# Optimization experiments

Measured on AMD Instinct MI355X. Metric: run time of the kernel, lower is better.

The kernel has to match this reference:

```python
import jax, jax.numpy as jnp
import numpy as np

R = 32            # voxel resolution
DIM = 240         # channels C
EPS_NORM = 0.0    # module eps
BN_EPS = 1e-5     # torch BatchNorm1d default eps


def setup_inputs() -> dict:
    key = jax.random.key(0)
    k1, k2, k3 = jax.random.split(key, 3)
    B, C, N = 4, DIM, 32768
    features = jax.random.normal(k1, (B, C, N), jnp.float32)
    coords = jax.random.uniform(k2, (B, 3, N), jnp.float32)
    # mlp params: Conv1d(2C -> C, kernel 1) + BatchNorm1d(C)
    w = jax.random.normal(k3, (C, 2 * C), jnp.float32) / np.sqrt(2 * C).astype(np.float32)
    b = jnp.zeros((C,), jnp.float32)
    gamma = jnp.ones((C,), jnp.float32)
    beta = jnp.zeros((C,), jnp.float32)
    return {"features": features, "coords": coords, "w": w, "b": b, "gamma": gamma, "beta": beta}


def _voxelize(features, coords):
    # normalize coords into [0, 1], scale to voxel grid
    nc = coords - coords.mean(axis=2, keepdims=True)                      # [B,3,N]
    scale = jnp.linalg.norm(nc, axis=1, keepdims=True).max(axis=2, keepdims=True) * 2.0 + EPS_NORM
    nc = nc / scale + 0.5
    nc = jnp.clip(nc * R, 0, R - 1)
    vox = jnp.round(nc).astype(jnp.int32)
    pos = vox[:, 0] + vox[:, 1] * R + vox[:, 2] * (R * R)                 # [B,N] flattened voxel id
    R3 = R * R * R

    def per_batch(f, p):
        # f: [C,N], p: [N] -> [2C, R3]; per-voxel max feature + second (min) feature
        mx = jax.ops.segment_max(f.T, p, num_segments=R3)                 # [R3, C]
        mn = jax.ops.segment_min(f.T, p, num_segments=R3)                 # [R3, C]
        cnt = jax.ops.segment_sum(jnp.ones_like(p), p, num_segments=R3)  # [R3]
        mask = (cnt > 0)[:, None]
        mx = jnp.where(mask, mx, 0.0)
        mn = jnp.where(mask, mn, 0.0)
        return jnp.concatenate([mx, mn], axis=1).T                        # [2C, R3]

    fea = jax.vmap(per_batch)(features, pos)                              # [B,2C,R3]
    return fea, nc


def reference(features, coords, w, b, gamma, beta):
    fea, nc = _voxelize(features, coords)
    # 1x1 Conv1d (pointwise GEMM) + BatchNorm1d (training-mode batch stats) + Swish
    y = jnp.einsum('co,bov->bcv', w, fea) + b[None, :, None]
    mean = y.mean(axis=(0, 2), keepdims=True)
    var = y.var(axis=(0, 2), keepdims=True)
    y = gamma[None, :, None] * (y - mean) * jax.lax.rsqrt(var + BN_EPS) + beta[None, :, None]
    y = y * jax.nn.sigmoid(y)
    B, C, _ = features.shape
    return y.reshape(B, C, R, R, R), nc
```

## Files before the change

### kernel.cpp

```cpp
#include <hip/hip_runtime.h>
#include <cstdint>
#include <cstddef>

#define RR 32
#define R3 32768
#define NPT 32768
#define CH 240
#define CH2 480
#define NB 4
#define Y_ELEMS 31457280

typedef __attribute__((ext_vector_type(8))) short short8v;
typedef __attribute__((ext_vector_type(4))) float float4v;

union u8pack { short8v v; unsigned short u[8]; };

static __device__ __forceinline__ float bf2f(unsigned short u) {
  return __uint_as_float(((unsigned int)u) << 16);
}
static __device__ __forceinline__ unsigned short f2bf(float f) {
  unsigned int u = __float_as_uint(f);
  u = (u + 0x7FFFu + ((u >> 16) & 1u)) >> 16;
  return (unsigned short)u;
}

__global__ void k_init(int* __restrict__ cnt, float* __restrict__ stats,
                       const float* __restrict__ w, unsigned short* __restrict__ wfrag) {
  int g = blockIdx.x * 256 + threadIdx.x;
  if (g < NB * R3) cnt[g] = 0;
  if (g < 1024) stats[g] = 0.0f;
  if (g < 14400) {
    int lane = g & 63, t = g >> 6;
    int mg = t / 75, r = t % 75;
    int kc = r / 5, mL = r % 5;
    int m = mg * 5 + mL;
    int ln = lane & 15, q = lane >> 4;
    const float* src = w + (size_t)(m * 16 + ln) * CH2 + kc * 32 + q * 8;
    u8pack pk;
#pragma unroll
    for (int j = 0; j < 8; j++) pk.u[j] = f2bf(src[j]);
    *(short8v*)&wfrag[(size_t)g * 8] = pk.v;
  }
}

__global__ __launch_bounds__(1024) void k_coord_stats(const float* __restrict__ coords,
                                                      float* __restrict__ ms) {
  __shared__ float red[1024];
  __shared__ float mean[3];
  int b = blockIdx.x, t = threadIdx.x;
  const float4* cb4 = (const float4*)(coords + (size_t)b * 3 * NPT);
  float s[3] = {0.f, 0.f, 0.f};
  for (int i = t; i < NPT / 4; i += 1024) {
#pragma unroll
    for (int d = 0; d < 3; d++) {
      float4 v = cb4[d * (NPT / 4) + i];
      s[d] += (v.x + v.y) + (v.z + v.w);
    }
  }
  for (int d = 0; d < 3; d++) {
    red[t] = s[d]; __syncthreads();
    for (int k = 512; k > 0; k >>= 1) { if (t < k) red[t] += red[t + k]; __syncthreads(); }
    if (t == 0) mean[d] = red[0] * (1.0f / NPT);
    __syncthreads();
  }
  float m0 = mean[0], m1 = mean[1], m2 = mean[2];
  float mx = 0.f;
  for (int i = t; i < NPT / 4; i += 1024) {
    float4 x = cb4[i], y = cb4[NPT / 4 + i], z = cb4[2 * (NPT / 4) + i];
    float dx, dy, dz, n;
    dx = x.x - m0; dy = y.x - m1; dz = z.x - m2; n = dx * dx + dy * dy + dz * dz; mx = fmaxf(mx, n);
    dx = x.y - m0; dy = y.y - m1; dz = z.y - m2; n = dx * dx + dy * dy + dz * dz; mx = fmaxf(mx, n);
    dx = x.z - m0; dy = y.z - m1; dz = z.z - m2; n = dx * dx + dy * dy + dz * dz; mx = fmaxf(mx, n);
    dx = x.w - m0; dy = y.w - m1; dz = z.w - m2; n = dx * dx + dy * dy + dz * dz; mx = fmaxf(mx, n);
  }
  red[t] = mx; __syncthreads();
  for (int k = 512; k > 0; k >>= 1) { if (t < k) red[t] = fmaxf(red[t], red[t + k]); __syncthreads(); }
  if (t == 0) {
    ms[b * 4 + 0] = m0; ms[b * 4 + 1] = m1; ms[b * 4 + 2] = m2;
    ms[b * 4 + 3] = sqrtf(red[0]) * 2.0f;
  }
}

__global__ void k_pos_nc(const float* __restrict__ coords, const float* __restrict__ ms,
                         float* __restrict__ ncout, int* __restrict__ pos, int* __restrict__ cnt) {
  int g = blockIdx.x * 256 + threadIdx.x;
  int b = g >> 15, i = g & (NPT - 1);
  const float* cb = coords + (size_t)b * 3 * NPT;
  float scale = ms[b * 4 + 3];
  int vox[3];
#pragma unroll
  for (int d = 0; d < 3; d++) {
    float v = (cb[(size_t)d * NPT + i] - ms[b * 4 + d]) / scale + 0.5f;
    v = fminf(fmaxf(v * (float)RR, 0.0f), (float)(RR - 1));
    ncout[((size_t)(b * 3 + d)) * NPT + i] = v;
    vox[d] = (int)rintf(v);
  }
  int p = (b << 15) | (vox[0] + (vox[1] << 5) + (vox[2] << 10));
  pos[g] = p;
  atomicAdd(&cnt[p], 1);
}

__global__ void k_scan(const int* __restrict__ cnt, int* __restrict__ offs) {
  __shared__ int part[1024];
  int b = blockIdx.x, t = threadIdx.x;
  const int base = b * R3;
  int local[32];
  int s = 0;
#pragma unroll
  for (int j = 0; j < 32; j++) { local[j] = cnt[base + t * 32 + j]; s += local[j]; }
  part[t] = s; __syncthreads();
  for (int d = 1; d < 1024; d <<= 1) {
    int v = (t >= d) ? part[t - d] : 0;
    __syncthreads();
    part[t] += v;
    __syncthreads();
  }
  int run = (t == 0) ? 0 : part[t - 1];
#pragma unroll
  for (int j = 0; j < 32; j++) { offs[base + t * 32 + j] = run; run += local[j]; }
}

__global__ void k_scatter(const int* __restrict__ pos, int* __restrict__ offs,
                          int* __restrict__ rank) {
  int g = blockIdx.x * 256 + threadIdx.x;
  int p = pos[g];
  int slot = atomicAdd(&offs[p], 1);
  rank[g] = slot;
}

__global__ void k_transpose3(const float* __restrict__ f, const int* __restrict__ rank,
                             unsigned short* __restrict__ fts) {
  __shared__ float tile[CH * 65];
  __shared__ int slts[64];
  int p0 = blockIdx.x * 64, b = blockIdx.y;
  int t = threadIdx.x;
  if (t < 64) slts[t] = rank[b * NPT + p0 + t];
  {
    int pp = t & 63, cq = t >> 6;
    const float* src = f + ((size_t)b * CH) * NPT + p0 + pp;
#pragma unroll 4
    for (int j = 0; j < 60; ++j) {
      int c = j * 4 + cq;
      tile[c * 65 + pp] = src[(size_t)c * NPT];
    }
  }
  __syncthreads();
  int ch8 = t & 7;
#pragma unroll
  for (int pass = 0; pass < 2; ++pass) {
    int p = pass * 32 + (t >> 3);
    unsigned short* dst = fts + ((size_t)(b * NPT + slts[p])) * CH;
#pragma unroll
    for (int i = 0; i < 4; ++i) {
      int ch = ch8 + 8 * i;
      if (ch < 30) {
        u8pack pk;
#pragma unroll
        for (int jj = 0; jj < 8; ++jj) pk.u[jj] = f2bf(tile[(ch * 8 + jj) * 65 + p]);
        *(short8v*)&dst[ch * 8] = pk.v;
      }
    }
  }
}

__global__ __launch_bounds__(512, 2) void k_fused(const int* __restrict__ cnt,
                                                  const int* __restrict__ offs,
                                                  const unsigned short* __restrict__ fts,
                                                  const unsigned short* __restrict__ wfrag,
                                                  const float* __restrict__ bias,
                                                  unsigned short* __restrict__ ybf,
                                                  float* __restrict__ gstats) {
  __shared__ unsigned short fB[8 * 15 * 512];
  __shared__ float bstats[480];
  int tid = threadIdx.x;
  int wave = tid >> 6, lane = tid & 63;
  int sub = lane >> 5, l = lane & 31;
  int ln = lane & 15, q = lane >> 4;
  int b = blockIdx.y;
  int v0 = blockIdx.x * 128;
  int bbase = b << 15;

  for (int i = tid; i < 480; i += 512) bstats[i] = 0.0f;

  int proc = wave * 2 + sub;
  int t1c = 30 + l;
  int kc0 = l >> 2, q0 = l & 3;
  int kc1 = t1c >> 2, q1 = t1c & 3;
#pragma unroll 1
  for (int it = 0; it < 8; ++it) {
    if (l < 30) {
      int v = bbase + v0 + it * 16 + proc;
      int ci0 = (q0 * 16 + proc) ^ ((kc0 & 3) << 1);
      int ci1 = (q1 * 16 + proc) ^ ((kc1 & 3) << 1);
      int idx0 = ((it * 15 + kc0) * 64 + ci0) * 8;
      int idx1 = ((it * 15 + kc1) * 64 + ci1) * 8;
      int n = cnt[v];
      if (n == 0) {
        u8pack z;
#pragma unroll
        for (int k = 0; k < 8; k++) z.u[k] = 0;
        *(short8v*)&fB[idx0] = z.v;
        *(short8v*)&fB[idx1] = z.v;
      } else {
        int start = offs[v] - n;
        const unsigned short* sp = fts + (size_t)(bbase + start) * CH + l * 8;
        float mx[8], mn[8];
#pragma unroll
        for (int k = 0; k < 8; k++) { mx[k] = -__builtin_inff(); mn[k] = __builtin_inff(); }
        int j = 0;
        for (; j + 4 <= n; j += 4) {
          u8pack u0, u1, u2, u3;
          u0.v = *(const short8v*)(sp);
          u1.v = *(const short8v*)(sp + CH);
          u2.v = *(const short8v*)(sp + 2 * CH);
          u3.v = *(const short8v*)(sp + 3 * CH);
          sp += 4 * CH;
#pragma unroll
          for (int k = 0; k < 8; k++) {
            float a0 = bf2f(u0.u[k]), a1 = bf2f(u1.u[k]);
            float a2 = bf2f(u2.u[k]), a3 = bf2f(u3.u[k]);
            mx[k] = fmaxf(mx[k], fmaxf(fmaxf(a0, a1), fmaxf(a2, a3)));
            mn[k] = fminf(mn[k], fminf(fminf(a0, a1), fminf(a2, a3)));
          }
        }
        for (; j < n; ++j) {
          u8pack u0;
          u0.v = *(const short8v*)(sp);
          sp += CH;
#pragma unroll
          for (int k = 0; k < 8; k++) {
            float a = bf2f(u0.u[k]);
            mx[k] = fmaxf(mx[k], a);
            mn[k] = fminf(mn[k], a);
          }
        }
        u8pack omx, omn;
#pragma unroll
        for (int k = 0; k < 8; k++) { omx.u[k] = f2bf(mx[k]); omn.u[k] = f2bf(mn[k]); }
        *(short8v*)&fB[idx0] = omx.v;
        *(short8v*)&fB[idx1] = omn.v;
      }
    }
  }

  int nmt = (wave == 7) ? 1 : 2;
  short8v wreg[2][15];
#pragma unroll
  for (int mm = 0; mm < 2; ++mm)
    if (mm < nmt) {
      int mt = wave * 2 + mm;
      int mg = mt / 5, mL = mt % 5;
      const unsigned short* wp = wfrag + ((size_t)(mg * 75 + mL) * 512) + lane * 8;
#pragma unroll
      for (int kc = 0; kc < 15; ++kc)
        wreg[mm][kc] = *(const short8v*)(wp + (size_t)kc * 5 * 512);
    }

  __syncthreads();

  float4v acc[2][8];
#pragma unroll
  for (int mm = 0; mm < 2; ++mm)
#pragma unroll
    for (int cg = 0; cg < 8; ++cg) acc[mm][cg] = (float4v){0.f, 0.f, 0.f, 0.f};

#pragma unroll
  for (int kc = 0; kc < 15; ++kc) {
    const unsigned short* fbl = fB + (size_t)((lane ^ ((kc & 3) << 1)) * 8);
    short8v bf[8];
#pragma unroll
    for (int cg = 0; cg < 8; ++cg)
      bf[cg] = *(const short8v*)(fbl + (size_t)(cg * 15 + kc) * 512);
#pragma unroll
    for (int mm = 0; mm < 2; ++mm)
      if (mm < nmt)
#pragma unroll
        for (int cg = 0; cg < 8; ++cg)
          acc[mm][cg] = __builtin_amdgcn_mfma_f32_16x16x32_bf16(wreg[mm][kc], bf[cg], acc[mm][cg], 0, 0, 0);
  }

  unsigned short* yb = ybf + ((size_t)b * CH) * R3 + v0 + ln;
#pragma unroll
  for (int mm = 0; mm < 2; ++mm)
    if (mm < nmt) {
      int mt = wave * 2 + mm;
#pragma unroll
      for (int r = 0; r < 4; ++r) {
        int c = mt * 16 + q * 4 + r;
        float bb = bias[c];
        unsigned short* yrow = yb + (size_t)c * R3;
        float s = 0.f, sq = 0.f;
#pragma unroll
        for (int cg = 0; cg < 8; ++cg) {
          float yv = acc[mm][cg][r] + bb;
          yrow[cg * 16] = f2bf(yv);
          s += yv; sq += yv * yv;
        }
#pragma unroll
        for (int off = 1; off < 16; off <<= 1) {
          s += __shfl_xor(s, off);
          sq += __shfl_xor(sq, off);
        }
        if (ln == 0) {
          atomicAdd(&bstats[c], s);
          atomicAdd(&bstats[240 + c], sq);
        }
      }
    }
  __syncthreads();
  for (int i = tid; i < 480; i += 512) {
    int g = (i < 240) ? i : (CH + (i - 240));
    atomicAdd(&gstats[g], bstats[i]);
  }
}

__global__ void k_apply(const unsigned short* __restrict__ ybf, float* __restrict__ out,
                        const float* __restrict__ stats, const float* __restrict__ gamma,
                        const float* __restrict__ beta) {
  int g = blockIdx.x * 256 + threadIdx.x;
  int c = (g >> 12) % CH;
  const float ninv = 1.0f / (float)(NB * R3);
  float mean = stats[c] * ninv;
  float var = stats[CH + c] * ninv - mean * mean;
  float s = gamma[c] * rsqrtf(var + 1e-5f);
  float h = beta[c] - mean * s;
  u8pack v;
  v.v = *(const short8v*)(ybf + (size_t)g * 8);
  float4 o0, o1;
  float t;
  t = bf2f(v.u[0]) * s + h; o0.x = t / (1.0f + __expf(-t));
  t = bf2f(v.u[1]) * s + h; o0.y = t / (1.0f + __expf(-t));
  t = bf2f(v.u[2]) * s + h; o0.z = t / (1.0f + __expf(-t));
  t = bf2f(v.u[3]) * s + h; o0.w = t / (1.0f + __expf(-t));
  t = bf2f(v.u[4]) * s + h; o1.x = t / (1.0f + __expf(-t));
  t = bf2f(v.u[5]) * s + h; o1.y = t / (1.0f + __expf(-t));
  t = bf2f(v.u[6]) * s + h; o1.z = t / (1.0f + __expf(-t));
  t = bf2f(v.u[7]) * s + h; o1.w = t / (1.0f + __expf(-t));
  ((float4*)out)[(size_t)g * 2] = o0;
  ((float4*)out)[(size_t)g * 2 + 1] = o1;
}

extern "C" void kernel_launch(void* const* d_in, const int* in_sizes, int n_in,
                              void* d_out, int out_size, void* d_ws, size_t ws_size,
                              hipStream_t stream) {
  const float* features = (const float*)d_in[0];
  const float* coords   = (const float*)d_in[1];
  const float* w        = (const float*)d_in[2];
  const float* bias     = (const float*)d_in[3];
  const float* gamma    = (const float*)d_in[4];
  const float* beta     = (const float*)d_in[5];
  float* out = (float*)d_out;

  char* ws = (char*)d_ws;
  size_t off = 0;
  float* ms    = (float*)(ws + off); off += 256;
  float* stats = (float*)(ws + off); off += 4096;
  int* pos     = (int*)(ws + off);   off += (size_t)NB * NPT * 4;
  int* cnt     = (int*)(ws + off);   off += (size_t)NB * R3 * 4;
  int* offs    = (int*)(ws + off);   off += (size_t)NB * R3 * 4;
  int* rank    = (int*)(ws + off);   off += (size_t)NB * NPT * 4;
  unsigned short* wfrag = (unsigned short*)(ws + off); off += (size_t)CH * CH2 * 2;
  unsigned short* fts   = (unsigned short*)(ws + off); off += (size_t)NB * NPT * CH * 2;
  unsigned short* ybf   = (unsigned short*)(ws + off); off += (size_t)NB * R3 * CH * 2;

  float* ncout = out + Y_ELEMS;

  k_init<<<516, 256, 0, stream>>>(cnt, stats, w, wfrag);
  k_coord_stats<<<4, 1024, 0, stream>>>(coords, ms);
  k_pos_nc<<<512, 256, 0, stream>>>(coords, ms, ncout, pos, cnt);
  k_scan<<<4, 1024, 0, stream>>>(cnt, offs);
  k_scatter<<<512, 256, 0, stream>>>(pos, offs, rank);
  k_transpose3<<<dim3(512, 4), 256, 0, stream>>>(features, rank, fts);
  k_fused<<<dim3(256, NB), 512, 0, stream>>>(cnt, offs, fts, wfrag, bias, ybf, stats);
  k_apply<<<Y_ELEMS / 2048, 256, 0, stream>>>(ybf, out, stats, gamma, beta);
}
```

Baseline: 394.8 us.

## Halve fused voxel tile, raise occupancy, stage counts in LDS, spread stat atomics

The fused reduce+GEMM kernel now handles 64 voxels per block instead of 128. That halves LDS and accumulator usage so four blocks can fit per CU, and the grid doubles. Voxel counts and offsets are preloaded into shared memory, and the gather loop is unrolled to 8 points with a 2-point tail. The LDS swizzle is changed, and the global BN stats atomics are spread over 8 slots that k_apply sums, which reduces atomic contention. The cost is reloading the weight fragments twice as often per voxel and a small extra reduction in the apply kernel.

```diff
diff --git a/kernel.cpp b/kernel.cpp
--- a/kernel.cpp
+++ b/kernel.cpp
@@ -28,7 +28,7 @@
                        const float* __restrict__ w, unsigned short* __restrict__ wfrag) {
   int g = blockIdx.x * 256 + threadIdx.x;
   if (g < NB * R3) cnt[g] = 0;
-  if (g < 1024) stats[g] = 0.0f;
+  if (g < 4096) stats[g] = 0.0f;
   if (g < 14400) {
     int lane = g & 63, t = g >> 6;
     int mg = t / 75, r = t % 75;
@@ -163,38 +163,43 @@
   }
 }
 
-__global__ __launch_bounds__(512, 2) void k_fused(const int* __restrict__ cnt,
+__global__ __launch_bounds__(512, 4) void k_fused(const int* __restrict__ cnt,
                                                   const int* __restrict__ offs,
                                                   const unsigned short* __restrict__ fts,
                                                   const unsigned short* __restrict__ wfrag,
                                                   const float* __restrict__ bias,
                                                   unsigned short* __restrict__ ybf,
                                                   float* __restrict__ gstats) {
-  __shared__ unsigned short fB[8 * 15 * 512];
+  __shared__ unsigned short fB[4 * 15 * 512];
   __shared__ float bstats[480];
+  __shared__ int scnt[64];
+  __shared__ int soffs[64];
   int tid = threadIdx.x;
   int wave = tid >> 6, lane = tid & 63;
   int sub = lane >> 5, l = lane & 31;
   int ln = lane & 15, q = lane >> 4;
   int b = blockIdx.y;
-  int v0 = blockIdx.x * 128;
+  int v0 = blockIdx.x * 64;
   int bbase = b << 15;
 
   for (int i = tid; i < 480; i += 512) bstats[i] = 0.0f;
+  if (tid < 64) scnt[tid] = cnt[bbase + v0 + tid];
+  else if (tid < 128) soffs[tid - 64] = offs[bbase + v0 + (tid - 64)];
+  __syncthreads();
 
   int proc = wave * 2 + sub;
   int t1c = 30 + l;
   int kc0 = l >> 2, q0 = l & 3;
   int kc1 = t1c >> 2, q1 = t1c & 3;
 #pragma unroll 1
-  for (int it = 0; it < 8; ++it) {
+  for (int it = 0; it < 4; ++it) {
     if (l < 30) {
-      int v = bbase + v0 + it * 16 + proc;
-      int ci0 = (q0 * 16 + proc) ^ ((kc0 & 3) << 1);
-      int ci1 = (q1 * 16 + proc) ^ ((kc1 & 3) << 1);
+      int lv = it * 16 + proc;
+      int ci0 = (q0 * 16 + proc) ^ (kc0 & 7);
+      int ci1 = (q1 * 16 + proc) ^ (kc1 & 7);
       int idx0 = ((it * 15 + kc0) * 64 + ci0) * 8;
       int idx1 = ((it * 15 + kc1) * 64 + ci1) * 8;
-      int n = cnt[v];
+      int n = scnt[lv];
       if (n == 0) {
         u8pack z;
 #pragma unroll
@@ -202,31 +207,52 @@
         *(short8v*)&fB[idx0] = z.v;
         *(short8v*)&fB[idx1] = z.v;
       } else {
-        int start = offs[v] - n;
+        int start = soffs[lv] - n;
         const unsigned short* sp = fts + (size_t)(bbase + start) * CH + l * 8;
         float mx[8], mn[8];
 #pragma unroll
         for (int k = 0; k < 8; k++) { mx[k] = -__builtin_inff(); mn[k] = __builtin_inff(); }
         int j = 0;
-        for (; j + 4 <= n; j += 4) {
-          u8pack u0, u1, u2, u3;
+        for (; j + 8 <= n; j += 8) {
+          u8pack u0, u1, u2, u3, u4, u5, u6, u7;
           u0.v = *(const short8v*)(sp);
           u1.v = *(const short8v*)(sp + CH);
           u2.v = *(const short8v*)(sp + 2 * CH);
           u3.v = *(const short8v*)(sp + 3 * CH);
-          sp += 4 * CH;
+          u4.v = *(const short8v*)(sp + 4 * CH);
+          u5.v = *(const short8v*)(sp + 5 * CH);
+          u6.v = *(const short8v*)(sp + 6 * CH);
+          u7.v = *(const short8v*)(sp + 7 * CH);
+          sp += 8 * CH;
 #pragma unroll
           for (int k = 0; k < 8; k++) {
             float a0 = bf2f(u0.u[k]), a1 = bf2f(u1.u[k]);
             float a2 = bf2f(u2.u[k]), a3 = bf2f(u3.u[k]);
-            mx[k] = fmaxf(mx[k], fmaxf(fmaxf(a0, a1), fmaxf(a2, a3)));
-            mn[k] = fminf(mn[k], fminf(fminf(a0, a1), fminf(a2, a3)));
+            float a4 = bf2f(u4.u[k]), a5 = bf2f(u5.u[k]);
+            float a6 = bf2f(u6.u[k]), a7 = bf2f(u7.u[k]);
+            float hx = fmaxf(fmaxf(fmaxf(a0, a1), fmaxf(a2, a3)),
+                             fmaxf(fmaxf(a4, a5), fmaxf(a6, a7)));
+            float hn = fminf(fminf(fminf(a0, a1), fminf(a2, a3)),
+                             fminf(fminf(a4, a5), fminf(a6, a7)));
+            mx[k] = fmaxf(mx[k], hx);
+            mn[k] = fminf(mn[k], hn);
           }
         }
-        for (; j < n; ++j) {
+        for (; j + 2 <= n; j += 2) {
+          u8pack u0, u1;
+          u0.v = *(const short8v*)(sp);
+          u1.v = *(const short8v*)(sp + CH);
+          sp += 2 * CH;
+#pragma unroll
+          for (int k = 0; k < 8; k++) {
+            float a0 = bf2f(u0.u[k]), a1 = bf2f(u1.u[k]);
+            mx[k] = fmaxf(mx[k], fmaxf(a0, a1));
+            mn[k] = fminf(mn[k], fminf(a0, a1));
+          }
+        }
+        if (j < n) {
           u8pack u0;
           u0.v = *(const short8v*)(sp);
-          sp += CH;
 #pragma unroll
           for (int k = 0; k < 8; k++) {
             float a = bf2f(u0.u[k]);
@@ -258,24 +284,24 @@
 
   __syncthreads();
 
-  float4v acc[2][8];
+  float4v acc[2][4];
 #pragma unroll
   for (int mm = 0; mm < 2; ++mm)
 #pragma unroll
-    for (int cg = 0; cg < 8; ++cg) acc[mm][cg] = (float4v){0.f, 0.f, 0.f, 0.f};
+    for (int cg = 0; cg < 4; ++cg) acc[mm][cg] = (float4v){0.f, 0.f, 0.f, 0.f};
 
 #pragma unroll
   for (int kc = 0; kc < 15; ++kc) {
-    const unsigned short* fbl = fB + (size_t)((lane ^ ((kc & 3) << 1)) * 8);
-    short8v bf[8];
-#pragma unroll
-    for (int cg = 0; cg < 8; ++cg)
+    const unsigned short* fbl = fB + (size_t)((lane ^ (kc & 7)) * 8);
+    short8v bf[4];
+#pragma unroll
+    for (int cg = 0; cg < 4; ++cg)
       bf[cg] = *(const short8v*)(fbl + (size_t)(cg * 15 + kc) * 512);
 #pragma unroll
     for (int mm = 0; mm < 2; ++mm)
       if (mm < nmt)
 #pragma unroll
-        for (int cg = 0; cg < 8; ++cg)
+        for (int cg = 0; cg < 4; ++cg)
           acc[mm][cg] = __builtin_amdgcn_mfma_f32_16x16x32_bf16(wreg[mm][kc], bf[cg], acc[mm][cg], 0, 0, 0);
   }
 
@@ -291,7 +317,7 @@
         unsigned short* yrow = yb + (size_t)c * R3;
         float s = 0.f, sq = 0.f;
 #pragma unroll
-        for (int cg = 0; cg < 8; ++cg) {
+        for (int cg = 0; cg < 4; ++cg) {
           float yv = acc[mm][cg][r] + bb;
           yrow[cg * 16] = f2bf(yv);
           s += yv; sq += yv * yv;
@@ -308,9 +334,10 @@
       }
     }
   __syncthreads();
+  float* gslot = gstats + (size_t)(blockIdx.x & 7) * 512;
   for (int i = tid; i < 480; i += 512) {
-    int g = (i < 240) ? i : (CH + (i - 240));
-    atomicAdd(&gstats[g], bstats[i]);
+    int g = (i < 240) ? i : (256 + (i - 240));
+    atomicAdd(&gslot[g], bstats[(i < 240) ? i : (240 + (i - 240))]);
   }
 }
 
@@ -320,8 +347,14 @@
   int g = blockIdx.x * 256 + threadIdx.x;
   int c = (g >> 12) % CH;
   const float ninv = 1.0f / (float)(NB * R3);
-  float mean = stats[c] * ninv;
-  float var = stats[CH + c] * ninv - mean * mean;
+  float sum = 0.f, ssq = 0.f;
+#pragma unroll
+  for (int sl = 0; sl < 8; ++sl) {
+    sum += stats[sl * 512 + c];
+    ssq += stats[sl * 512 + 256 + c];
+  }
+  float mean = sum * ninv;
+  float var = ssq * ninv - mean * mean;
   float s = gamma[c] * rsqrtf(var + 1e-5f);
   float h = beta[c] - mean * s;
   u8pack v;
@@ -354,7 +387,7 @@
   char* ws = (char*)d_ws;
   size_t off = 0;
   float* ms    = (float*)(ws + off); off += 256;
-  float* stats = (float*)(ws + off); off += 4096;
+  float* stats = (float*)(ws + off); off += 16384;
   int* pos     = (int*)(ws + off);   off += (size_t)NB * NPT * 4;
   int* cnt     = (int*)(ws + off);   off += (size_t)NB * R3 * 4;
   int* offs    = (int*)(ws + off);   off += (size_t)NB * R3 * 4;
@@ -371,6 +404,6 @@
   k_scan<<<4, 1024, 0, stream>>>(cnt, offs);
   k_scatter<<<512, 256, 0, stream>>>(pos, offs, rank);
   k_transpose3<<<dim3(512, 4), 256, 0, stream>>>(features, rank, fts);
-  k_fused<<<dim3(256, NB), 512, 0, stream>>>(cnt, offs, fts, wfrag, bias, ybf, stats);
+  k_fused<<<dim3(512, NB), 512, 0, stream>>>(cnt, offs, fts, wfrag, bias, ybf, stats);
   k_apply<<<Y_ELEMS / 2048, 256, 0, stream>>>(ybf, out, stats, gamma, beta);
 }
```

New measurement: 426.8 us. +8.1%, slower.
